# Optimization experiments

Hardware: AMD Instinct MI355X
Metric: run time of the kernel (lower is better)

## Reference

```python
import jax, jax.numpy as jnp
import numpy as np

N = 50000      # nodes
E = 800000     # edges (before self-loops)
F_IN = 512     # input features
H = 8          # heads (layer 1)
C = 32         # hidden per head
CLS = 40       # classes


def setup_inputs() -> dict:
    key = jax.random.key(0)
    ks = jax.random.split(key, 10)
    small = lambda k, shape: jax.random.normal(k, shape, jnp.float32) * 0.05
    return {
        "x": jax.random.normal(ks[0], (N, F_IN), jnp.float32),
        "edge_index": jax.random.randint(ks[1], (2, E), 0, N, jnp.int32),
        # layer 1 params (GATConv: F_IN -> C per head, 8 heads, concat)
        "W1": small(ks[2], (F_IN, H * C)),
        "a_src1": small(ks[3], (H, C)),
        "a_dst1": small(ks[4], (H, C)),
        "b1": jnp.zeros((H * C,), jnp.float32),
        # layer 2 params (GATConv: H*C -> CLS, 1 head)
        "W2": small(ks[5], (H * C, CLS)),
        "a_src2": small(ks[6], (1, CLS)),
        "a_dst2": small(ks[7], (1, CLS)),
        "b2": jnp.zeros((CLS,), jnp.float32),
    }


def gat_conv(x, W, a_src, a_dst, b, src, dst, n):
    """PyG-style GATConv (negative_slope=0.2); self-loops already in src/dst."""
    h_, c_ = a_src.shape
    h = (x @ W).reshape(n, h_, c_)                       # [N, H, C]
    alpha_src = jnp.einsum('nhc,hc->nh', h, a_src)       # [N, H]
    alpha_dst = jnp.einsum('nhc,hc->nh', h, a_dst)       # [N, H]
    e = jax.nn.leaky_relu(alpha_src[src] + alpha_dst[dst], 0.2)  # [E', H]
    # segment softmax over incoming edges of each destination node
    m = jax.lax.stop_gradient(jax.ops.segment_max(e, dst, num_segments=n))
    ex = jnp.exp(e - m[dst])
    den = jax.ops.segment_sum(ex, dst, num_segments=n)
    alpha = ex / (den[dst] + 1e-16)                      # [E', H]
    out = jax.ops.segment_sum(h[src] * alpha[:, :, None], dst, num_segments=n)
    return out.reshape(n, h_ * c_) + b


def reference(x, edge_index, W1, a_src1, a_dst1, b1, W2, a_src2, a_dst2, b2):
    n = x.shape[0]
    loop = jnp.arange(n, dtype=edge_index.dtype)
    src = jnp.concatenate([edge_index[0], loop])  # add self-loops (PyG default)
    dst = jnp.concatenate([edge_index[1], loop])
    # dropout is identity at inference
    h = jax.nn.elu(gat_conv(x, W1, a_src1, a_dst1, b1, src, dst, n))
    out = gat_conv(h, W2, a_src2, a_dst2, b2, src, dst, n)
    return jax.nn.log_softmax(out, axis=1)
```

## Files before the change

### kernel.cpp

```cpp
#include <hip/hip_runtime.h>
#include <hip/hip_bf16.h>
#include <math.h>

constexpr int NN  = 50000;
constexpr int NE  = 800000;
constexpr int EP  = NE + NN;
constexpr int FIN = 512;
constexpr int NH  = 8;
constexpr int NC  = 32;
constexpr int HC  = NH * NC;
constexpr int CLS = 40;
constexpr int CLSP = 48;
constexpr int NGB = (NN + 63) / 64;
constexpr int NSB = 1024;

typedef __attribute__((ext_vector_type(8))) __bf16 bf16x8;
typedef __attribute__((ext_vector_type(4))) __bf16 bf16x4;
typedef __attribute__((ext_vector_type(4))) float f32x4;
typedef __attribute__((ext_vector_type(2))) float f32x2;

__device__ inline bf16x8 cvt8(const float4 a, const float4 b) {
  bf16x8 o;
  o[0] = (__bf16)a.x; o[1] = (__bf16)a.y; o[2] = (__bf16)a.z; o[3] = (__bf16)a.w;
  o[4] = (__bf16)b.x; o[5] = (__bf16)b.y; o[6] = (__bf16)b.z; o[7] = (__bf16)b.w;
  return o;
}

__device__ inline bf16x8 cvt8v(const f32x4 a, const f32x4 b) {
  bf16x8 o;
  o[0] = (__bf16)a.x; o[1] = (__bf16)a.y; o[2] = (__bf16)a.z; o[3] = (__bf16)a.w;
  o[4] = (__bf16)b.x; o[5] = (__bf16)b.y; o[6] = (__bf16)b.z; o[7] = (__bf16)b.w;
  return o;
}

__device__ inline unsigned char to_fp8(float f) {
  int pk = __builtin_amdgcn_cvt_pk_fp8_f32(f, f, 0, false);
  return (unsigned char)(pk & 0xff);
}

__global__ void k_hist(const int* __restrict__ ei, int* __restrict__ deg) {
  int e = blockIdx.x * 256 + threadIdx.x;
  if (e >= EP) return;
  int d = (e < NE) ? ei[NE + e] : (e - NE);
  atomicAdd(&deg[d], 1);
}

__global__ __launch_bounds__(1024) void k_scan1(const int* __restrict__ deg,
                                                int* __restrict__ rowptr1,
                                                int* __restrict__ bsum, int n) {
  __shared__ int sm[1024];
  int i = blockIdx.x * 1024 + threadIdx.x;
  int v = (i < n) ? deg[i] : 0;
  sm[threadIdx.x] = v;
  __syncthreads();
  for (int off = 1; off < 1024; off <<= 1) {
    int t = (threadIdx.x >= off) ? sm[threadIdx.x - off] : 0;
    __syncthreads();
    sm[threadIdx.x] += t;
    __syncthreads();
  }
  if (i < n) rowptr1[i] = sm[threadIdx.x];
  if (threadIdx.x == 1023) bsum[blockIdx.x] = sm[1023];
}

__global__ void k_scan2(int* __restrict__ bsum, int nb) {
  int lane = threadIdx.x;
  int v = (lane < nb) ? bsum[lane] : 0;
#pragma unroll
  for (int off = 1; off < 64; off <<= 1) {
    int t = __shfl_up(v, off);
    if (lane >= off) v += t;
  }
  int ex = __shfl_up(v, 1);
  if (lane == 0) ex = 0;
  if (lane < nb) bsum[lane] = ex;
}

__global__ void k_scan3(int* __restrict__ rowptr, const int* __restrict__ bsum,
                        int* __restrict__ cursor, int n) {
  int i = blockIdx.x * 256 + threadIdx.x;
  if (i == 0) { rowptr[0] = 0; cursor[0] = 0; }
  if (i < n) {
    int v = rowptr[i + 1] + bsum[i >> 10];
    rowptr[i + 1] = v;
    if (i + 1 < n) cursor[i + 1] = v;
  }
}

__global__ void k_cvt_w(const float* __restrict__ W1, const float* __restrict__ W2,
                        __bf16* __restrict__ Wt, __bf16* __restrict__ W2t) {
  int t = blockIdx.x * 256 + threadIdx.x;
  if (t < HC * (FIN / 8)) {
    int c = t >> 6, kq = (t & 63) * 8;
    bf16x8 o;
#pragma unroll
    for (int j = 0; j < 8; ++j) o[j] = (__bf16)W1[(size_t)(kq + j) * HC + c];
    *(bf16x8*)&Wt[(size_t)c * FIN + kq] = o;
  } else {
    int u = t - HC * (FIN / 8);
    if (u < CLSP * HC) {
      int c = u >> 8, k = u & 255;
      W2t[u] = (c < CLS) ? (__bf16)W2[(size_t)k * CLS + c] : (__bf16)0.f;
    }
  }
}

__global__ __launch_bounds__(256) void k_gemm1_scatter(
    const float* __restrict__ X, const __bf16* __restrict__ Wt,
    const float* __restrict__ a_s1, const float* __restrict__ a_d1,
    unsigned char* __restrict__ Hout, float* __restrict__ asrc1,
    float* __restrict__ adst1,
    const int* __restrict__ ei, int* __restrict__ cursor,
    unsigned short* __restrict__ srcS) {
  __shared__ __align__(16) float Xp[2][4096];
  const int tid = threadIdx.x;

  if (blockIdx.x >= NGB) {
    int base = (blockIdx.x - NGB) * 256 + tid;
    for (int e = base; e < EP; e += NSB * 256) {
      int s, d;
      if (e < NE) { s = ei[e]; d = ei[NE + e]; } else { s = d = e - NE; }
      int p = atomicAdd(&cursor[d], 1);
      srcS[p] = (unsigned short)s;
    }
    return;
  }

  const int lane = tid & 63;
  const int w    = tid >> 6;
  const int wn   = w * 64;
  const int bm   = blockIdx.x * 64;
  const int l15  = lane & 15, lg = lane >> 4;

  const int srow_l  = (lane >> 4);
  const int sslot   = (l15 >> 1);
  const int shalf   = (lane & 1);

  f32x4 acc[4][4] = {};

  auto issue = [&](int c, int buf) {
#pragma unroll
    for (int jj = 0; jj < 4; ++jj) {
      const int j = w * 4 + jj;
      const int row_l = 4 * j + srow_l;
      const int rowG = min(bm + row_l, NN - 1);
      const int g = sslot ^ (row_l & 7);
      const float* src = X + (size_t)rowG * FIN + c * 64 + g * 8 + shalf * 4;
      __builtin_amdgcn_global_load_lds(
          (const __attribute__((address_space(1))) void*)src,
          (__attribute__((address_space(3))) void*)(&Xp[buf][j * 256]), 16, 0, 0);
    }
  };

  issue(0, 0);
  for (int c = 0; c < 8; ++c) {
    const int cur = c & 1;
    __syncthreads();
    if (c < 7) issue(c + 1, cur ^ 1);

#pragma unroll
    for (int kh = 0; kh < 2; ++kh) {
      const int kb = lg + 4 * kh;
      bf16x8 bv[4];
#pragma unroll
      for (int ni = 0; ni < 4; ++ni)
        bv[ni] = *(const bf16x8*)(Wt + (size_t)(wn + ni * 16 + l15) * FIN
                                     + c * 64 + kb * 8);
#pragma unroll
      for (int mi = 0; mi < 4; ++mi) {
        int r = mi * 16 + l15;
        int fo = r * 64 + ((kb ^ (r & 7)) << 3);
        f32x4 alo = *(const f32x4*)&Xp[cur][fo];
        f32x4 ahi = *(const f32x4*)&Xp[cur][fo + 4];
        bf16x8 av = cvt8v(alo, ahi);
#pragma unroll
        for (int ni = 0; ni < 4; ++ni)
          acc[mi][ni] = __builtin_amdgcn_mfma_f32_16x16x32_bf16(
              av, bv[ni], acc[mi][ni], 0, 0, 0);
      }
    }
    __syncthreads();
  }

  const int hbase = 2 * w;
#pragma unroll
  for (int hh = 0; hh < 2; ++hh) {
    float asA = a_s1[(hbase + hh) * NC + l15];
    float asB = a_s1[(hbase + hh) * NC + 16 + l15];
    float adA = a_d1[(hbase + hh) * NC + l15];
    float adB = a_d1[(hbase + hh) * NC + 16 + l15];
    float vs = 0.f, vd = 0.f;
#pragma unroll
    for (int mi = 0; mi < 4; ++mi) {
#pragma unroll
      for (int r = 0; r < 4; ++r) {
        float ps = acc[mi][2 * hh][r] * asA + acc[mi][2 * hh + 1][r] * asB;
        float pd = acc[mi][2 * hh][r] * adA + acc[mi][2 * hh + 1][r] * adB;
#pragma unroll
        for (int off = 1; off < 16; off <<= 1) {
          ps += __shfl_xor(ps, off, 64);
          pd += __shfl_xor(pd, off, 64);
        }
        if (l15 == mi * 4 + r) { vs = ps; vd = pd; }
      }
    }
    int rw = bm + (l15 >> 2) * 16 + lg * 4 + (l15 & 3);
    if (rw < NN) {
      asrc1[(size_t)rw * NH + hbase + hh] = vs;
      adst1[(size_t)rw * NH + hbase + hh] = vd;
    }
  }

#pragma unroll
  for (int mi = 0; mi < 4; ++mi) {
#pragma unroll
    for (int ni = 0; ni < 4; ++ni) {
      int col = wn + ni * 16 + l15;
#pragma unroll
      for (int r = 0; r < 4; ++r) {
        int row = bm + mi * 16 + lg * 4 + r;
        if (row < NN) Hout[(size_t)row * HC + col] = to_fp8(acc[mi][ni][r]);
      }
    }
  }
}

__global__ __launch_bounds__(256) void k_agg1(const unsigned char* __restrict__ h1f8,
                                              const float* __restrict__ asrc,
                                              const float* __restrict__ adst,
                                              const unsigned short* __restrict__ srcS,
                                              const int* __restrict__ rowptr,
                                              const float* __restrict__ b1,
                                              __bf16* __restrict__ helu) {
  int wave = (blockIdx.x * 256 + threadIdx.x) >> 6;
  int lane = threadIdx.x & 63;
  if (wave >= NN) return;
  int lo = rowptr[wave], hi = rowptr[wave + 1];
  int head = lane >> 3;
  int hw   = lane & 7;
  float adstv = adst[wave * NH + head];
  float ad2   = adst[wave * NH + hw];
  float4 acc = {0.f, 0.f, 0.f, 0.f};
  float den = 0.f;

  for (int base = lo; base < hi; base += 64) {
    int cnt = hi - base; if (cnt > 64) cnt = 64;
    int sv = (lane < cnt) ? (int)srcS[base + lane] : 0;
    int j = 0;
    for (; j + 8 <= cnt; j += 8) {
      int se = __shfl(sv, j + head);
      float v = asrc[se * NH + hw] + ad2;
      v = v > 0.f ? v : 0.2f * v;
      float wv = __expf(v);
      int s[8]; unsigned int hv[8];
#pragma unroll
      for (int u = 0; u < 8; ++u) s[u] = __shfl(sv, j + u);
#pragma unroll
      for (int u = 0; u < 8; ++u)
        hv[u] = *(const unsigned int*)&h1f8[(size_t)s[u] * HC + lane * 4];
#pragma unroll
      for (int u = 0; u < 8; ++u) {
        float wu = __shfl(wv, u * 8 + head);
        f32x2 lo2 = __builtin_amdgcn_cvt_pk_f32_fp8(hv[u], false);
        f32x2 hi2 = __builtin_amdgcn_cvt_pk_f32_fp8(hv[u], true);
        acc.x += wu * lo2.x;
        acc.y += wu * lo2.y;
        acc.z += wu * hi2.x;
        acc.w += wu * hi2.y;
        den += wu;
      }
    }
    for (; j < cnt; ++j) {
      int s = __shfl(sv, j);
      float v = asrc[s * NH + head] + adstv;
      v = v > 0.f ? v : 0.2f * v;
      float w = __expf(v);
      unsigned int hv = *(const unsigned int*)&h1f8[(size_t)s * HC + lane * 4];
      f32x2 lo2 = __builtin_amdgcn_cvt_pk_f32_fp8(hv, false);
      f32x2 hi2 = __builtin_amdgcn_cvt_pk_f32_fp8(hv, true);
      acc.x += w * lo2.x;
      acc.y += w * lo2.y;
      acc.z += w * hi2.x;
      acc.w += w * hi2.y;
      den += w;
    }
  }

  float inv = 1.f / (den + 1e-16f);
  float4 bb = *(const float4*)&b1[lane * 4];
  float o[4] = {acc.x * inv + bb.x, acc.y * inv + bb.y,
                acc.z * inv + bb.z, acc.w * inv + bb.w};
  bf16x4 ov;
#pragma unroll
  for (int j2 = 0; j2 < 4; ++j2) {
    float e = o[j2] > 0.f ? o[j2] : expm1f(o[j2]);
    ov[j2] = (__bf16)e;
  }
  *(bf16x4*)&helu[(size_t)wave * HC + lane * 4] = ov;
}

__global__ __launch_bounds__(256) void k_gemm2m(const __bf16* __restrict__ A,
                                                const __bf16* __restrict__ W2t,
                                                const float* __restrict__ a_s2,
                                                const float* __restrict__ a_d2,
                                                __bf16* __restrict__ Hout,
                                                float* __restrict__ asrc2,
                                                float* __restrict__ adst2) {
  __shared__ __align__(16) __bf16 As[128 * 8 * 8];
  __shared__ __align__(16) __bf16 Bsh[CLSP * 33 * 8];
  const int tid  = threadIdx.x;
  const int lane = tid & 63;
  const int w    = tid >> 6;
  const int wm   = w * 32;
  const int bm   = blockIdx.x * 128;

  const int l3 = lane >> 3;
  const int l7 = lane & 7;
  const int kb_src = l7 ^ l3;

  for (int s = tid; s < CLSP * 32; s += 256) {
    int c = s >> 5, kb = s & 31;
    *(bf16x8*)(Bsh + (size_t)(c * 33 + kb) * 8) =
        *(const bf16x8*)(W2t + (size_t)c * HC + kb * 8);
  }

  f32x4 acc[2][3] = {};

  for (int step = 0; step < 4; ++step) {
    const int k0 = step * 64;
#pragma unroll
    for (int q = 0; q < 4; ++q) {
      const int inst = w * 4 + q;
      const int r = inst * 8 + l3;
      const int arow = min(bm + r, NN - 1);
      const __bf16* ga = A + (size_t)arow * HC + k0 + kb_src * 8;
      __builtin_amdgcn_global_load_lds(
          (const __attribute__((address_space(1))) void*)ga,
          (__attribute__((address_space(3))) void*)(As + inst * 512), 16, 0, 0);
    }
    __syncthreads();

    const int l15 = lane & 15, lg = lane >> 4;
#pragma unroll
    for (int kh = 0; kh < 2; ++kh) {
      const int kbl = lg + 4 * kh;
      const int kbg = step * 8 + kbl;
      bf16x8 av[2], bv[3];
#pragma unroll
      for (int mi = 0; mi < 2; ++mi) {
        int r = wm + mi * 16 + l15;
        av[mi] = *(const bf16x8*)(As + (size_t)(r * 8 + (kbl ^ (r & 7))) * 8);
      }
#pragma unroll
      for (int ni = 0; ni < 3; ++ni) {
        int c = ni * 16 + l15;
        bv[ni] = *(const bf16x8*)(Bsh + (size_t)(c * 33 + kbg) * 8);
      }
#pragma unroll
      for (int mi = 0; mi < 2; ++mi)
#pragma unroll
        for (int ni = 0; ni < 3; ++ni)
          acc[mi][ni] = __builtin_amdgcn_mfma_f32_16x16x32_bf16(
              av[mi], bv[ni], acc[mi][ni], 0, 0, 0);
    }
    __syncthreads();
  }

  const int l15 = lane & 15, lg = lane >> 4;

  {
    int c0 = l15, c1 = 16 + l15, c2 = 32 + l15;
    float as0 = a_s2[c0], as1 = a_s2[c1], as2v = (c2 < CLS) ? a_s2[c2] : 0.f;
    float ad0 = a_d2[c0], ad1 = a_d2[c1], ad2v = (c2 < CLS) ? a_d2[c2] : 0.f;
    float vs = 0.f, vd = 0.f;
#pragma unroll
    for (int mi = 0; mi < 2; ++mi) {
#pragma unroll
      for (int r = 0; r < 4; ++r) {
        float ps = acc[mi][0][r] * as0 + acc[mi][1][r] * as1 + acc[mi][2][r] * as2v;
        float pd = acc[mi][0][r] * ad0 + acc[mi][1][r] * ad1 + acc[mi][2][r] * ad2v;
#pragma unroll
        for (int off = 1; off < 16; off <<= 1) {
          ps += __shfl_xor(ps, off, 64);
          pd += __shfl_xor(pd, off, 64);
        }
        if (l15 == mi * 4 + r) { vs = ps; vd = pd; }
      }
    }
    int rw = bm + wm + (l15 >> 2) * 16 + lg * 4 + (l15 & 3);
    if (l15 < 8 && rw < NN) {
      asrc2[rw] = vs;
      adst2[rw] = vd;
    }
  }

#pragma unroll
  for (int mi = 0; mi < 2; ++mi) {
#pragma unroll
    for (int ni = 0; ni < 3; ++ni) {
      int col = ni * 16 + l15;
      if (col >= CLS) continue;
#pragma unroll
      for (int r = 0; r < 4; ++r) {
        int row = bm + wm + mi * 16 + lg * 4 + r;
        if (row < NN) Hout[(size_t)row * CLS + col] = (__bf16)acc[mi][ni][r];
      }
    }
  }
}

__global__ __launch_bounds__(256) void k_agg2(const __bf16* __restrict__ h2b,
                                              const float* __restrict__ asrc,
                                              const float* __restrict__ adst,
                                              const unsigned short* __restrict__ srcS,
                                              const int* __restrict__ rowptr,
                                              const float* __restrict__ b2,
                                              float* __restrict__ out) {
  int wave = (blockIdx.x * 256 + threadIdx.x) >> 6;
  int lane = threadIdx.x & 63;
  if (wave >= NN) return;
  int lo = rowptr[wave], hi = rowptr[wave + 1];
  bool act = lane < CLS;
  float adstv = adst[wave];
  float acc = 0.f, den = 0.f;

  for (int base = lo; base < hi; base += 64) {
    int cnt = hi - base; if (cnt > 64) cnt = 64;
    int sv = (lane < cnt) ? (int)srcS[base + lane] : 0;
    float v = asrc[sv] + adstv;
    v = v > 0.f ? v : 0.2f * v;
    float wv = __expf(v);
    int j = 0;
    for (; j + 8 <= cnt; j += 8) {
      int s[8]; float hval[8];
#pragma unroll
      for (int u = 0; u < 8; ++u) s[u] = __shfl(sv, j + u);
#pragma unroll
      for (int u = 0; u < 8; ++u)
        hval[u] = act ? (float)h2b[(size_t)s[u] * CLS + lane] : 0.f;
#pragma unroll
      for (int u = 0; u < 8; ++u) {
        float wu = __shfl(wv, j + u);
        acc += wu * hval[u];
        den += wu;
      }
    }
    for (; j < cnt; ++j) {
      int s = __shfl(sv, j);
      float wu = __shfl(wv, j);
      if (act) acc += wu * (float)h2b[(size_t)s * CLS + lane];
      den += wu;
    }
  }

  float o = act ? (acc / (den + 1e-16f) + b2[lane]) : -INFINITY;
  float m = o;
#pragma unroll
  for (int off = 32; off; off >>= 1) m = fmaxf(m, __shfl_xor(m, off, 64));
  float ex = act ? __expf(o - m) : 0.f;
  float ssum = ex;
#pragma unroll
  for (int off = 32; off; off >>= 1) ssum += __shfl_xor(ssum, off, 64);
  if (act) out[(size_t)wave * CLS + lane] = o - m - logf(ssum);
}

extern "C" void kernel_launch(void* const* d_in, const int* in_sizes, int n_in,
                              void* d_out, int out_size, void* d_ws, size_t ws_size,
                              hipStream_t stream) {
  const float* x      = (const float*)d_in[0];
  const int*   ei     = (const int*)d_in[1];
  const float* W1     = (const float*)d_in[2];
  const float* a_src1 = (const float*)d_in[3];
  const float* a_dst1 = (const float*)d_in[4];
  const float* b1     = (const float*)d_in[5];
  const float* W2     = (const float*)d_in[6];
  const float* a_src2 = (const float*)d_in[7];
  const float* a_dst2 = (const float*)d_in[8];
  const float* b2     = (const float*)d_in[9];
  float* out = (float*)d_out;

  char* p = (char*)d_ws;
  auto alloc = [&](size_t bytes) {
    char* r = p;
    p += (bytes + 255) & ~size_t(255);
    return r;
  };
  unsigned char* h1f8 = (unsigned char*)alloc((size_t)NN * HC);
  __bf16* helu  = (__bf16*)alloc((size_t)NN * HC * 2);
  __bf16* Wt    = (__bf16*)alloc((size_t)HC * FIN * 2);
  __bf16* W2t   = (__bf16*)alloc((size_t)CLSP * HC * 2);
  __bf16* h2b   = (__bf16*)alloc((size_t)NN * CLS * 2);
  float*  asrc1 = (float*)alloc((size_t)NN * NH * 4);
  float*  adst1 = (float*)alloc((size_t)NN * NH * 4);
  float*  asrc2 = (float*)alloc((size_t)NN * 4);
  float*  adst2 = (float*)alloc((size_t)NN * 4);
  unsigned short* srcS = (unsigned short*)alloc((size_t)EP * 2);
  int*    deg   = (int*)alloc((size_t)NN * 4);
  int*    cursor= (int*)alloc((size_t)NN * 4);
  int*    rowptr= (int*)alloc((size_t)(NN + 1) * 4);
  int*    bsum  = (int*)alloc(256 * 4);

  hipMemsetAsync(deg, 0, (size_t)NN * 4, stream);

  const int nbScan = (NN + 1023) / 1024;
  k_hist<<<(EP + 255) / 256, 256, 0, stream>>>(ei, deg);
  k_scan1<<<nbScan, 1024, 0, stream>>>(deg, rowptr + 1, bsum, NN);
  k_scan2<<<1, 64, 0, stream>>>(bsum, nbScan);
  k_scan3<<<(NN + 255) / 256, 256, 0, stream>>>(rowptr, bsum, cursor, NN);

  k_cvt_w<<<(HC * (FIN / 8) + CLSP * HC + 255) / 256, 256, 0, stream>>>(W1, W2, Wt, W2t);

  k_gemm1_scatter<<<NGB + NSB, 256, 0, stream>>>(x, Wt, a_src1, a_dst1,
                                                 h1f8, asrc1, adst1,
                                                 ei, cursor, srcS);

  k_agg1<<<(NN + 3) / 4, 256, 0, stream>>>(h1f8, asrc1, adst1, srcS, rowptr, b1, helu);

  k_gemm2m<<<(NN + 127) / 128, 256, 0, stream>>>(helu, W2t, a_src2, a_dst2,
                                                 h2b, asrc2, adst2);
  k_agg2<<<(NN + 3) / 4, 256, 0, stream>>>(h2b, asrc2, adst2, srcS, rowptr, b2, out);
}
```

Before: 231.6 us.

## Merge histogram and weight conversion; store layer-2 features as padded fp8

Folds the degree histogram and the weight transpose/convert into one prep launch, which removes a kernel launch. The edge-scatter blocks in the GEMM1 kernel now get one block per 256 edges instead of a fixed 1024 blocks with a grid-stride loop. Layer-2 projected features are stored as fp8 in 64-byte padded rows instead of bf16, which cuts the gather bytes in the second aggregation at some cost in precision.

```diff
diff --git a/kernel.cpp b/kernel.cpp
--- a/kernel.cpp
+++ b/kernel.cpp
@@ -12,19 +12,14 @@
 constexpr int CLS = 40;
 constexpr int CLSP = 48;
 constexpr int NGB = (NN + 63) / 64;
-constexpr int NSB = 1024;
+constexpr int NSCB = (EP + 255) / 256;
+constexpr int CVTW_ITEMS = HC * (FIN / 8) + CLSP * HC;
+constexpr int CVTW_B = (CVTW_ITEMS + 255) / 256;
 
 typedef __attribute__((ext_vector_type(8))) __bf16 bf16x8;
 typedef __attribute__((ext_vector_type(4))) __bf16 bf16x4;
 typedef __attribute__((ext_vector_type(4))) float f32x4;
 typedef __attribute__((ext_vector_type(2))) float f32x2;
-
-__device__ inline bf16x8 cvt8(const float4 a, const float4 b) {
-  bf16x8 o;
-  o[0] = (__bf16)a.x; o[1] = (__bf16)a.y; o[2] = (__bf16)a.z; o[3] = (__bf16)a.w;
-  o[4] = (__bf16)b.x; o[5] = (__bf16)b.y; o[6] = (__bf16)b.z; o[7] = (__bf16)b.w;
-  return o;
-}
 
 __device__ inline bf16x8 cvt8v(const f32x4 a, const f32x4 b) {
   bf16x8 o;
@@ -38,11 +33,33 @@
   return (unsigned char)(pk & 0xff);
 }
 
-__global__ void k_hist(const int* __restrict__ ei, int* __restrict__ deg) {
-  int e = blockIdx.x * 256 + threadIdx.x;
-  if (e >= EP) return;
-  int d = (e < NE) ? ei[NE + e] : (e - NE);
-  atomicAdd(&deg[d], 1);
+__device__ inline float from_fp8(unsigned char b) {
+  f32x2 v = __builtin_amdgcn_cvt_pk_f32_fp8((unsigned)b, false);
+  return v.x;
+}
+
+__global__ void k_prep(const int* __restrict__ ei, int* __restrict__ deg,
+                       const float* __restrict__ W1, const float* __restrict__ W2,
+                       __bf16* __restrict__ Wt, __bf16* __restrict__ W2t) {
+  if (blockIdx.x < NSCB) {
+    int e = blockIdx.x * 256 + threadIdx.x;
+    if (e >= EP) return;
+    int d = (e < NE) ? ei[NE + e] : (e - NE);
+    atomicAdd(&deg[d], 1);
+    return;
+  }
+  int t = (blockIdx.x - NSCB) * 256 + threadIdx.x;
+  if (t < HC * (FIN / 8)) {
+    int c = t >> 6, kq = (t & 63) * 8;
+    bf16x8 o;
+#pragma unroll
+    for (int j = 0; j < 8; ++j) o[j] = (__bf16)W1[(size_t)(kq + j) * HC + c];
+    *(bf16x8*)&Wt[(size_t)c * FIN + kq] = o;
+  } else if (t < CVTW_ITEMS) {
+    int u = t - HC * (FIN / 8);
+    int c = u >> 8, k = u & 255;
+    W2t[u] = (c < CLS) ? (__bf16)W2[(size_t)k * CLS + c] : (__bf16)0.f;
+  }
 }
 
 __global__ __launch_bounds__(1024) void k_scan1(const int* __restrict__ deg,
@@ -87,24 +104,6 @@
   }
 }
 
-__global__ void k_cvt_w(const float* __restrict__ W1, const float* __restrict__ W2,
-                        __bf16* __restrict__ Wt, __bf16* __restrict__ W2t) {
-  int t = blockIdx.x * 256 + threadIdx.x;
-  if (t < HC * (FIN / 8)) {
-    int c = t >> 6, kq = (t & 63) * 8;
-    bf16x8 o;
-#pragma unroll
-    for (int j = 0; j < 8; ++j) o[j] = (__bf16)W1[(size_t)(kq + j) * HC + c];
-    *(bf16x8*)&Wt[(size_t)c * FIN + kq] = o;
-  } else {
-    int u = t - HC * (FIN / 8);
-    if (u < CLSP * HC) {
-      int c = u >> 8, k = u & 255;
-      W2t[u] = (c < CLS) ? (__bf16)W2[(size_t)k * CLS + c] : (__bf16)0.f;
-    }
-  }
-}
-
 __global__ __launch_bounds__(256) void k_gemm1_scatter(
     const float* __restrict__ X, const __bf16* __restrict__ Wt,
     const float* __restrict__ a_s1, const float* __restrict__ a_d1,
@@ -116,8 +115,8 @@
   const int tid = threadIdx.x;
 
   if (blockIdx.x >= NGB) {
-    int base = (blockIdx.x - NGB) * 256 + tid;
-    for (int e = base; e < EP; e += NSB * 256) {
+    int e = (blockIdx.x - NGB) * 256 + tid;
+    if (e < EP) {
       int s, d;
       if (e < NE) { s = ei[e]; d = ei[NE + e]; } else { s = d = e - NE; }
       int p = atomicAdd(&cursor[d], 1);
@@ -303,7 +302,7 @@
                                                 const __bf16* __restrict__ W2t,
                                                 const float* __restrict__ a_s2,
                                                 const float* __restrict__ a_d2,
-                                                __bf16* __restrict__ Hout,
+                                                unsigned char* __restrict__ h2p,
                                                 float* __restrict__ asrc2,
                                                 float* __restrict__ adst2) {
   __shared__ __align__(16) __bf16 As[128 * 8 * 8];
@@ -403,13 +402,13 @@
 #pragma unroll
       for (int r = 0; r < 4; ++r) {
         int row = bm + wm + mi * 16 + lg * 4 + r;
-        if (row < NN) Hout[(size_t)row * CLS + col] = (__bf16)acc[mi][ni][r];
-      }
-    }
-  }
-}
-
-__global__ __launch_bounds__(256) void k_agg2(const __bf16* __restrict__ h2b,
+        if (row < NN) h2p[(size_t)row * 64 + col] = to_fp8(acc[mi][ni][r]);
+      }
+    }
+  }
+}
+
+__global__ __launch_bounds__(256) void k_agg2(const unsigned char* __restrict__ h2p,
                                               const float* __restrict__ asrc,
                                               const float* __restrict__ adst,
                                               const unsigned short* __restrict__ srcS,
@@ -437,7 +436,7 @@
       for (int u = 0; u < 8; ++u) s[u] = __shfl(sv, j + u);
 #pragma unroll
       for (int u = 0; u < 8; ++u)
-        hval[u] = act ? (float)h2b[(size_t)s[u] * CLS + lane] : 0.f;
+        hval[u] = act ? from_fp8(h2p[(size_t)s[u] * 64 + lane]) : 0.f;
 #pragma unroll
       for (int u = 0; u < 8; ++u) {
         float wu = __shfl(wv, j + u);
@@ -448,7 +447,7 @@
     for (; j < cnt; ++j) {
       int s = __shfl(sv, j);
       float wu = __shfl(wv, j);
-      if (act) acc += wu * (float)h2b[(size_t)s * CLS + lane];
+      if (act) acc += wu * from_fp8(h2p[(size_t)s * 64 + lane]);
       den += wu;
     }
   }
@@ -489,7 +488,7 @@
   __bf16* helu  = (__bf16*)alloc((size_t)NN * HC * 2);
   __bf16* Wt    = (__bf16*)alloc((size_t)HC * FIN * 2);
   __bf16* W2t   = (__bf16*)alloc((size_t)CLSP * HC * 2);
-  __bf16* h2b   = (__bf16*)alloc((size_t)NN * CLS * 2);
+  unsigned char* h2p = (unsigned char*)alloc((size_t)NN * 64);
   float*  asrc1 = (float*)alloc((size_t)NN * NH * 4);
   float*  adst1 = (float*)alloc((size_t)NN * NH * 4);
   float*  asrc2 = (float*)alloc((size_t)NN * 4);
@@ -503,20 +502,19 @@
   hipMemsetAsync(deg, 0, (size_t)NN * 4, stream);
 
   const int nbScan = (NN + 1023) / 1024;
-  k_hist<<<(EP + 255) / 256, 256, 0, stream>>>(ei, deg);
+  k_prep<<<NSCB + CVTW_B, 256, 0, stream>>>(ei, deg, W1, W2, Wt, W2t);
   k_scan1<<<nbScan, 1024, 0, stream>>>(deg, rowptr + 1, bsum, NN);
   k_scan2<<<1, 64, 0, stream>>>(bsum, nbScan);
   k_scan3<<<(NN + 255) / 256, 256, 0, stream>>>(rowptr, bsum, cursor, NN);
 
-  k_cvt_w<<<(HC * (FIN / 8) + CLSP * HC + 255) / 256, 256, 0, stream>>>(W1, W2, Wt, W2t);
-
-  k_gemm1_scatter<<<NGB + NSB, 256, 0, stream>>>(x, Wt, a_src1, a_dst1,
-                                                 h1f8, asrc1, adst1,
-                                                 ei, cursor, srcS);
+  k_gemm1_scatter<<<NGB + NSCB, 256, 0, stream>>>(x, Wt, a_src1, a_dst1,
+                                                  h1f8, asrc1, adst1,
+                                                  ei, cursor, srcS);
 
   k_agg1<<<(NN + 3) / 4, 256, 0, stream>>>(h1f8, asrc1, adst1, srcS, rowptr, b1, helu);
 
   k_gemm2m<<<(NN + 127) / 128, 256, 0, stream>>>(helu, W2t, a_src2, a_dst2,
-                                                 h2b, asrc2, adst2);
-  k_agg2<<<(NN + 3) / 4, 256, 0, stream>>>(h2b, asrc2, adst2, srcS, rowptr, b2, out);
-}
+                                                 h2p, asrc2, adst2);
+
+  k_agg2<<<(NN + 3) / 4, 256, 0, stream>>>(h2p, asrc2, adst2, srcS, rowptr, b2, out);
+}
```

New measurement: 226.3 us. 2.3% less time.
